# Kernel tuning notes

Measured on AMD Instinct MI355X. Metric: run time of the kernel, lower is better.

The kernel has to match this reference:

```python
import jax, jax.numpy as jnp
import numpy as np

B, N, DIM, H = 2, 2048, 1024, 16
D = DIM // H  # head_dim = 64


def setup_inputs() -> dict:
    key = jax.random.key(0)
    k1, k2, k3, k4, k5 = jax.random.split(key, 5)
    x = jax.random.normal(k1, (B, N, DIM), dtype=jnp.float32)
    # nn.Linear weights: [out_features, in_features]; scaled for stable softmax
    qkv_w = jax.random.normal(k2, (3 * DIM, DIM), dtype=jnp.float32) * (DIM ** -0.5)
    qkv_b = jax.random.normal(k3, (3 * DIM,), dtype=jnp.float32) * 0.02
    proj_w = jax.random.normal(k4, (DIM, DIM), dtype=jnp.float32) * (DIM ** -0.5)
    proj_b = jax.random.normal(k5, (DIM,), dtype=jnp.float32) * 0.02
    return {"x": x, "qkv_w": qkv_w, "qkv_b": qkv_b, "proj_w": proj_w, "proj_b": proj_b}


def reference(x, qkv_w, qkv_b, proj_w, proj_b):
    b, n, c = x.shape
    # qkv linear: [B,N,3C] -> [B,N,3,H,D] -> q,k,v each [B,H,N,D]
    qkv = x @ qkv_w.T + qkv_b
    qkv = qkv.reshape(b, n, 3, H, D).transpose(2, 0, 3, 1, 4)
    q, k, v = qkv[0], qkv[1], qkv[2]
    # scaled dot-product attention (no dropout, no mask); qk_norm=False, rope=None
    scale = D ** -0.5
    scores = jnp.einsum("bhqd,bhkd->bhqk", q, k) * scale
    attn = jax.nn.softmax(scores, axis=-1)
    out = jnp.einsum("bhqk,bhkd->bhqd", attn, v)
    # [B,H,N,D] -> [B,N,C]
    out = out.transpose(0, 2, 1, 3).reshape(b, n, c)
    # output projection
    return out @ proj_w.T + proj_b
```

## Files before the change

### kernel.cpp

```cpp
#include <hip/hip_runtime.h>
#include <hip/hip_bf16.h>
#include <math.h>

typedef __attribute__((ext_vector_type(8))) short short8v;
typedef __attribute__((ext_vector_type(4))) float f32x4;
typedef unsigned short ushort_t;

__device__ __forceinline__ ushort_t to_bf16(float v) {
    __hip_bfloat16 h = __float2bfloat16(v);
    return *(ushort_t*)&h;
}

__device__ __forceinline__ unsigned cvt_pk_bf16(float a, float b) {
    unsigned r;
    asm("v_cvt_pk_bf16_f32 %0, %1, %2" : "=v"(r) : "v"(a), "v"(b));
    return r;
}

__device__ __forceinline__ void load_lds_16B(const void* g, void* l) {
    __builtin_amdgcn_global_load_lds(
        (__attribute__((address_space(1))) unsigned int*)(g),
        (__attribute__((address_space(3))) unsigned int*)(l), 16, 0, 0);
}

__global__ __launch_bounds__(256) void convert_kernel(
    const float* __restrict__ x, const float* __restrict__ wq,
    const float* __restrict__ wp, ushort_t* __restrict__ xb,
    ushort_t* __restrict__ wqb, ushort_t* __restrict__ wpb)
{
    int c = blockIdx.x * 256 + threadIdx.x;
    const float* src; ushort_t* dst; int base;
    if (c < 524288)      { src = x;  dst = xb;  base = c; }
    else if (c < 917504) { src = wq; dst = wqb; base = c - 524288; }
    else                 { src = wp; dst = wpb; base = c - 917504; }
    const float4* s4 = (const float4*)src;
    float4 a = s4[2 * (size_t)base], b = s4[2 * (size_t)base + 1];
    float vals[8] = {a.x, a.y, a.z, a.w, b.x, b.y, b.z, b.w};
    short8v o;
#pragma unroll
    for (int j = 0; j < 8; j++) o[j] = (short)to_bf16(vals[j]);
    *(short8v*)(dst + 8 * (size_t)base) = o;
}

template <int MODE, int BM, int BN>
__global__ __launch_bounds__(256) void gemm_bf16_kernel(
    const ushort_t* __restrict__ A, const ushort_t* __restrict__ Bw,
    const float* __restrict__ bias, ushort_t* __restrict__ Qb,
    ushort_t* __restrict__ Kb, ushort_t* __restrict__ Vt,
    float* __restrict__ Cout)
{
    constexpr int MT = BM / 32, NT = BN / 32;
    __shared__ __align__(16) ushort_t As[BM * 32];
    __shared__ __align__(16) ushort_t Bs[BN * 32];
    const int t = threadIdx.x;
    const int w = t >> 6, l = t & 63;
    const int lo = l & 15, hi = l >> 4;
    const int wr = w >> 1, wc = w & 1;
    const int m0 = blockIdx.y * BM, n0 = blockIdx.x * BN;
    const int K = 1024;

    const ushort_t* ga = A + (size_t)(m0 + (t >> 2)) * K + (t & 3) * 8;
    const ushort_t* gb = Bw + (size_t)(n0 + (t >> 2)) * K + (t & 3) * 8;

    f32x4 acc[MT][NT] = {};

    for (int k0 = 0; k0 < 1024; k0 += 32) {
#pragma unroll
        for (int i = 0; i < BM / 64; i++)
            load_lds_16B(ga + (size_t)(i * 64) * K + k0, As + (i * 256 + w * 64) * 8);
#pragma unroll
        for (int i = 0; i < BN / 64; i++)
            load_lds_16B(gb + (size_t)(i * 64) * K + k0, Bs + (i * 256 + w * 64) * 8);
        __syncthreads();

        short8v af[MT], bf[NT];
#pragma unroll
        for (int mt = 0; mt < MT; mt++) {
            int r = wr * (BM / 2) + mt * 16 + lo;
            af[mt] = *(const short8v*)&As[r * 32 + hi * 8];
        }
#pragma unroll
        for (int nt = 0; nt < NT; nt++) {
            int r = wc * (BN / 2) + nt * 16 + lo;
            bf[nt] = *(const short8v*)&Bs[r * 32 + hi * 8];
        }
#pragma unroll
        for (int mt = 0; mt < MT; mt++)
#pragma unroll
            for (int nt = 0; nt < NT; nt++)
                acc[mt][nt] = __builtin_amdgcn_mfma_f32_16x16x32_bf16(
                    af[mt], bf[nt], acc[mt][nt], 0, 0, 0);
        __syncthreads();
    }

#pragma unroll
    for (int mt = 0; mt < MT; mt++) {
#pragma unroll
        for (int nt = 0; nt < NT; nt++) {
            int col = n0 + wc * (BN / 2) + nt * 16 + lo;
            float bv = bias[col];
#pragma unroll
            for (int reg = 0; reg < 4; reg++) {
                int row = m0 + wr * (BM / 2) + mt * 16 + hi * 4 + reg;
                float val = acc[mt][nt][reg] + bv;
                if constexpr (MODE == 0) {
                    int bb = row >> 11, n = row & 2047;
                    int which = col >> 10, rem = col & 1023;
                    int h = rem >> 6, d = rem & 63;
                    int bh = bb * 16 + h;
                    if (which == 0)
                        Qb[((size_t)bh * 2048 + n) * 64 + d] = to_bf16(val * 0.1803368601f);
                    else if (which == 1)
                        Kb[((size_t)bh * 2048 + n) * 64 + d] = to_bf16(val);
                    else
                        Vt[((size_t)bh * 64 + d) * 2048 + n] = to_bf16(val);
                } else {
                    Cout[(size_t)row * 1024 + col] = val;
                }
            }
        }
    }
}

__global__ __launch_bounds__(256) void attn_mfma_kernel(
    const ushort_t* __restrict__ Qg0, const ushort_t* __restrict__ Kg0,
    const ushort_t* __restrict__ Vg0, ushort_t* __restrict__ O)
{
    __shared__ __align__(16) ushort_t Ks[2 * 64 * 64];
    __shared__ __align__(16) ushort_t Vs[2 * 64 * 64];
    __shared__ __align__(16) ushort_t Ps[64 * 64];

    const int t = threadIdx.x;
    const int l = t & 63, w = t >> 6;
    const int lo = l & 15, hi = l >> 4;
    const int lin = (blockIdx.x & 7) * 128 + (blockIdx.x >> 3);
    const int bh = lin >> 5;
    const int q0 = (lin & 31) * 64;
    const ushort_t* Qg = Qg0 + (size_t)bh * 2048 * 64;
    const ushort_t* Kg = Kg0 + (size_t)bh * 2048 * 64;
    const ushort_t* Vg = Vg0 + (size_t)bh * 64 * 2048;

    short8v aq[2];
    {
        const ushort_t* qrow = Qg + (size_t)(q0 + w * 16 + lo) * 64;
        aq[0] = *(const short8v*)(qrow + hi * 8);
        aq[1] = *(const short8v*)(qrow + 32 + hi * 8);
    }

    const int srow = t >> 3, sg = t & 7;
    const int sgs = sg ^ (srow & 7);
    short8v rk0, rk1, rv0, rv1;

    f32x4 o_acc[4] = {};
    float m_i = -INFINITY, l_i = 0.0f;

    {
        rk0 = *(const short8v*)(Kg + (size_t)srow * 64 + sg * 8);
        rk1 = *(const short8v*)(Kg + (size_t)(srow + 32) * 64 + sg * 8);
        rv0 = *(const short8v*)(Vg + (size_t)srow * 2048 + sg * 8);
        rv1 = *(const short8v*)(Vg + (size_t)(srow + 32) * 2048 + sg * 8);
        *(short8v*)&Ks[srow * 64 + sgs * 8] = rk0;
        *(short8v*)&Ks[(srow + 32) * 64 + sgs * 8] = rk1;
        *(short8v*)&Vs[srow * 64 + sgs * 8] = rv0;
        *(short8v*)&Vs[(srow + 32) * 64 + sgs * 8] = rv1;
    }
    __syncthreads();

    for (int kt = 0; kt < 32; kt++) {
        const int bufo = (kt & 1) * 4096;
        if (kt < 31) {
            const int k0n = (kt + 1) * 64;
            rk0 = *(const short8v*)(Kg + (size_t)(k0n + srow) * 64 + sg * 8);
            rk1 = *(const short8v*)(Kg + (size_t)(k0n + srow + 32) * 64 + sg * 8);
            rv0 = *(const short8v*)(Vg + (size_t)srow * 2048 + k0n + sg * 8);
            rv1 = *(const short8v*)(Vg + (size_t)(srow + 32) * 2048 + k0n + sg * 8);
        }

        f32x4 s_acc[4];
        __builtin_amdgcn_s_setprio(1);
#pragma unroll
        for (int nt = 0; nt < 4; nt++) {
            f32x4 acc = {0.f, 0.f, 0.f, 0.f};
#pragma unroll
            for (int kk = 0; kk < 2; kk++) {
                int r = nt * 16 + lo;
                int g = (kk * 4 + hi) ^ (r & 7);
                short8v ak = *(const short8v*)&Ks[bufo + r * 64 + g * 8];
                acc = __builtin_amdgcn_mfma_f32_16x16x32_bf16(ak, aq[kk], acc, 0, 0, 0);
            }
            s_acc[nt] = acc;
        }
        __builtin_amdgcn_s_setprio(0);

        float pmax = fmaxf(
            fmaxf(fmaxf(fmaxf(s_acc[0][0], s_acc[0][1]), fmaxf(s_acc[0][2], s_acc[0][3])),
                  fmaxf(fmaxf(s_acc[1][0], s_acc[1][1]), fmaxf(s_acc[1][2], s_acc[1][3]))),
            fmaxf(fmaxf(fmaxf(s_acc[2][0], s_acc[2][1]), fmaxf(s_acc[2][2], s_acc[2][3])),
                  fmaxf(fmaxf(s_acc[3][0], s_acc[3][1]), fmaxf(s_acc[3][2], s_acc[3][3]))));
        pmax = fmaxf(pmax, __shfl_xor(pmax, 16));
        pmax = fmaxf(pmax, __shfl_xor(pmax, 32));

        if (__any(pmax > m_i + 11.0f)) {
            float mnew = fmaxf(m_i, pmax);
            float al = __builtin_amdgcn_exp2f(m_i - mnew);
            m_i = mnew;
            l_i *= al;
            float a0 = __shfl(al, hi * 4 + 0);
            float a1 = __shfl(al, hi * 4 + 1);
            float a2 = __shfl(al, hi * 4 + 2);
            float a3 = __shfl(al, hi * 4 + 3);
#pragma unroll
            for (int dt = 0; dt < 4; dt++) {
                o_acc[dt][0] *= a0; o_acc[dt][1] *= a1;
                o_acc[dt][2] *= a2; o_acc[dt][3] *= a3;
            }
        }

        float p[4][4];
        float ps = 0.0f;
#pragma unroll
        for (int nt = 0; nt < 4; nt++)
#pragma unroll
            for (int reg = 0; reg < 4; reg++) {
                p[nt][reg] = __builtin_amdgcn_exp2f(s_acc[nt][reg] - m_i);
                ps += p[nt][reg];
            }
        ps += __shfl_xor(ps, 16);
        ps += __shfl_xor(ps, 32);
        l_i += ps;

        const int R = w * 16 + lo;
#pragma unroll
        for (int nt = 0; nt < 4; nt++) {
            int c0 = nt * 16 + hi * 4;
            int g = (c0 >> 3) ^ (R & 7);
            uint2 pv = {cvt_pk_bf16(p[nt][0], p[nt][1]),
                        cvt_pk_bf16(p[nt][2], p[nt][3])};
            *(uint2*)&Ps[R * 64 + g * 8 + (c0 & 7)] = pv;
        }
        asm volatile("s_waitcnt lgkmcnt(0)" ::: "memory");
        short8v pa0 = *(const short8v*)&Ps[R * 64 + ((0 + hi) ^ (R & 7)) * 8];
        short8v pa1 = *(const short8v*)&Ps[R * 64 + ((4 + hi) ^ (R & 7)) * 8];

        if (kt < 31) {
            const int nxto = 4096 - bufo;
            *(short8v*)&Ks[nxto + srow * 64 + sgs * 8] = rk0;
            *(short8v*)&Ks[nxto + (srow + 32) * 64 + sgs * 8] = rk1;
            *(short8v*)&Vs[nxto + srow * 64 + sgs * 8] = rv0;
            *(short8v*)&Vs[nxto + (srow + 32) * 64 + sgs * 8] = rv1;
        }

        __builtin_amdgcn_s_setprio(1);
#pragma unroll
        for (int dt = 0; dt < 4; dt++) {
            int r = dt * 16 + lo;
            short8v bv0 = *(const short8v*)&Vs[bufo + r * 64 + ((0 + hi) ^ (r & 7)) * 8];
            short8v bv1 = *(const short8v*)&Vs[bufo + r * 64 + ((4 + hi) ^ (r & 7)) * 8];
            o_acc[dt] = __builtin_amdgcn_mfma_f32_16x16x32_bf16(pa0, bv0, o_acc[dt], 0, 0, 0);
            o_acc[dt] = __builtin_amdgcn_mfma_f32_16x16x32_bf16(pa1, bv1, o_acc[dt], 0, 0, 0);
        }
        __builtin_amdgcn_s_setprio(0);
        __syncthreads();
    }

    const int b = bh >> 4, h = bh & 15;
#pragma unroll
    for (int reg = 0; reg < 4; reg++) {
        float lv = __shfl(l_i, hi * 4 + reg);
        float inv = 1.0f / lv;
        int row = q0 + w * 16 + hi * 4 + reg;
        ushort_t* orow = O + ((size_t)(b * 2048 + row)) * 1024 + h * 64;
#pragma unroll
        for (int dt = 0; dt < 4; dt++)
            orow[dt * 16 + lo] = to_bf16(o_acc[dt][reg] * inv);
    }
}

extern "C" void kernel_launch(void* const* d_in, const int* in_sizes, int n_in,
                              void* d_out, int out_size, void* d_ws, size_t ws_size,
                              hipStream_t stream) {
    const float* x      = (const float*)d_in[0];
    const float* qkv_w  = (const float*)d_in[1];
    const float* qkv_b  = (const float*)d_in[2];
    const float* proj_w = (const float*)d_in[3];
    const float* proj_b = (const float*)d_in[4];
    float* out = (float*)d_out;

    ushort_t* xb  = (ushort_t*)d_ws;
    ushort_t* wqb = xb  + 4194304;
    ushort_t* wpb = wqb + 3145728;
    ushort_t* qb  = wpb + 1048576;
    ushort_t* kb  = qb  + 4194304;
    ushort_t* vt  = kb  + 4194304;
    ushort_t* aob = vt  + 4194304;

    convert_kernel<<<4096, 256, 0, stream>>>(x, qkv_w, proj_w, xb, wqb, wpb);
    gemm_bf16_kernel<0, 128, 128><<<dim3(24, 32), 256, 0, stream>>>(
        xb, wqb, qkv_b, qb, kb, vt, nullptr);
    attn_mfma_kernel<<<1024, 256, 0, stream>>>(qb, kb, vt, aob);
    gemm_bf16_kernel<1, 128, 128><<<dim3(8, 32), 256, 0, stream>>>(
        aob, wpb, proj_b, nullptr, nullptr, nullptr, out);
}
```

Baseline: 142.6 us.

## Double GEMM K-tile with swizzled LDS; keep P in registers via permuted V layout

The GEMM kernel now stages 64-wide K tiles in LDS with an XOR swizzle, which halves the number of barrier-separated iterations and reduces bank conflicts. The attention kernel drops the LDS round-trip for the softmax probabilities P. The bf16-packed P values are used directly as MFMA A operands, and V is written to LDS in a permuted, swizzled order so its key dimension lines up with the register layout P already has. This removes an LDS store, a wait and two reads per tile, at the cost of more complex V store addressing using 8-byte writes.

```diff
diff --git a/kernel.cpp b/kernel.cpp
--- a/kernel.cpp
+++ b/kernel.cpp
@@ -50,8 +50,8 @@
     float* __restrict__ Cout)
 {
     constexpr int MT = BM / 32, NT = BN / 32;
-    __shared__ __align__(16) ushort_t As[BM * 32];
-    __shared__ __align__(16) ushort_t Bs[BN * 32];
+    __shared__ __align__(16) ushort_t As[BM * 64];
+    __shared__ __align__(16) ushort_t Bs[BN * 64];
     const int t = threadIdx.x;
     const int w = t >> 6, l = t & 63;
     const int lo = l & 15, hi = l >> 4;
@@ -59,37 +59,45 @@
     const int m0 = blockIdx.y * BM, n0 = blockIdx.x * BN;
     const int K = 1024;
 
-    const ushort_t* ga = A + (size_t)(m0 + (t >> 2)) * K + (t & 3) * 8;
-    const ushort_t* gb = Bw + (size_t)(n0 + (t >> 2)) * K + (t & 3) * 8;
+    const int srow = t >> 3;
+    const int schk = (t & 7) ^ (srow & 7);
+    const ushort_t* ga = A + (size_t)(m0 + srow) * K + schk * 8;
+    const ushort_t* gb = Bw + (size_t)(n0 + srow) * K + schk * 8;
 
     f32x4 acc[MT][NT] = {};
 
-    for (int k0 = 0; k0 < 1024; k0 += 32) {
-#pragma unroll
-        for (int i = 0; i < BM / 64; i++)
-            load_lds_16B(ga + (size_t)(i * 64) * K + k0, As + (i * 256 + w * 64) * 8);
-#pragma unroll
-        for (int i = 0; i < BN / 64; i++)
-            load_lds_16B(gb + (size_t)(i * 64) * K + k0, Bs + (i * 256 + w * 64) * 8);
+    for (int k0 = 0; k0 < 1024; k0 += 64) {
+#pragma unroll
+        for (int i = 0; i < BM / 32; i++)
+            load_lds_16B(ga + (size_t)(i * 32) * K + k0, As + (i * 32 + w * 8) * 64);
+#pragma unroll
+        for (int i = 0; i < BN / 32; i++)
+            load_lds_16B(gb + (size_t)(i * 32) * K + k0, Bs + (i * 32 + w * 8) * 64);
         __syncthreads();
 
-        short8v af[MT], bf[NT];
+        short8v af[MT][2], bf[NT][2];
 #pragma unroll
         for (int mt = 0; mt < MT; mt++) {
             int r = wr * (BM / 2) + mt * 16 + lo;
-            af[mt] = *(const short8v*)&As[r * 32 + hi * 8];
+#pragma unroll
+            for (int kk = 0; kk < 2; kk++)
+                af[mt][kk] = *(const short8v*)&As[r * 64 + ((kk * 4 + hi) ^ (r & 7)) * 8];
         }
 #pragma unroll
         for (int nt = 0; nt < NT; nt++) {
             int r = wc * (BN / 2) + nt * 16 + lo;
-            bf[nt] = *(const short8v*)&Bs[r * 32 + hi * 8];
-        }
-#pragma unroll
-        for (int mt = 0; mt < MT; mt++)
-#pragma unroll
-            for (int nt = 0; nt < NT; nt++)
-                acc[mt][nt] = __builtin_amdgcn_mfma_f32_16x16x32_bf16(
-                    af[mt], bf[nt], acc[mt][nt], 0, 0, 0);
+#pragma unroll
+            for (int kk = 0; kk < 2; kk++)
+                bf[nt][kk] = *(const short8v*)&Bs[r * 64 + ((kk * 4 + hi) ^ (r & 7)) * 8];
+        }
+#pragma unroll
+        for (int kk = 0; kk < 2; kk++)
+#pragma unroll
+            for (int mt = 0; mt < MT; mt++)
+#pragma unroll
+                for (int nt = 0; nt < NT; nt++)
+                    acc[mt][nt] = __builtin_amdgcn_mfma_f32_16x16x32_bf16(
+                        af[mt][kk], bf[nt][kk], acc[mt][nt], 0, 0, 0);
         __syncthreads();
     }
 
@@ -128,7 +136,6 @@
 {
     __shared__ __align__(16) ushort_t Ks[2 * 64 * 64];
     __shared__ __align__(16) ushort_t Vs[2 * 64 * 64];
-    __shared__ __align__(16) ushort_t Ps[64 * 64];
 
     const int t = threadIdx.x;
     const int l = t & 63, w = t >> 6;
@@ -149,20 +156,27 @@
 
     const int srow = t >> 3, sg = t & 7;
     const int sgs = sg ^ (srow & 7);
-    short8v rk0, rk1, rv0, rv1;
+    const int gv0 = (sg >> 2) * 4 + (sg & 1) * 2;
+    const int vo = ((sg >> 1) & 1) * 4;
+    const int vswz0 = srow & 7;
+    uint4 rk0, rk1, rv0, rv1;
 
     f32x4 o_acc[4] = {};
     float m_i = -INFINITY, l_i = 0.0f;
 
     {
-        rk0 = *(const short8v*)(Kg + (size_t)srow * 64 + sg * 8);
-        rk1 = *(const short8v*)(Kg + (size_t)(srow + 32) * 64 + sg * 8);
-        rv0 = *(const short8v*)(Vg + (size_t)srow * 2048 + sg * 8);
-        rv1 = *(const short8v*)(Vg + (size_t)(srow + 32) * 2048 + sg * 8);
-        *(short8v*)&Ks[srow * 64 + sgs * 8] = rk0;
-        *(short8v*)&Ks[(srow + 32) * 64 + sgs * 8] = rk1;
-        *(short8v*)&Vs[srow * 64 + sgs * 8] = rv0;
-        *(short8v*)&Vs[(srow + 32) * 64 + sgs * 8] = rv1;
+        rk0 = *(const uint4*)(Kg + (size_t)srow * 64 + sg * 8);
+        rk1 = *(const uint4*)(Kg + (size_t)(srow + 32) * 64 + sg * 8);
+        rv0 = *(const uint4*)(Vg + (size_t)srow * 2048 + sg * 8);
+        rv1 = *(const uint4*)(Vg + (size_t)(srow + 32) * 2048 + sg * 8);
+        *(uint4*)&Ks[srow * 64 + sgs * 8] = rk0;
+        *(uint4*)&Ks[(srow + 32) * 64 + sgs * 8] = rk1;
+        uint2 a0 = {rv0.x, rv0.y}, b0 = {rv0.z, rv0.w};
+        uint2 a1 = {rv1.x, rv1.y}, b1 = {rv1.z, rv1.w};
+        *(uint2*)&Vs[srow * 64 + (gv0 ^ vswz0) * 8 + vo] = a0;
+        *(uint2*)&Vs[srow * 64 + ((gv0 + 1) ^ vswz0) * 8 + vo] = b0;
+        *(uint2*)&Vs[(srow + 32) * 64 + (gv0 ^ vswz0) * 8 + vo] = a1;
+        *(uint2*)&Vs[(srow + 32) * 64 + ((gv0 + 1) ^ vswz0) * 8 + vo] = b1;
     }
     __syncthreads();
 
@@ -170,10 +184,10 @@
         const int bufo = (kt & 1) * 4096;
         if (kt < 31) {
             const int k0n = (kt + 1) * 64;
-            rk0 = *(const short8v*)(Kg + (size_t)(k0n + srow) * 64 + sg * 8);
-            rk1 = *(const short8v*)(Kg + (size_t)(k0n + srow + 32) * 64 + sg * 8);
-            rv0 = *(const short8v*)(Vg + (size_t)srow * 2048 + k0n + sg * 8);
-            rv1 = *(const short8v*)(Vg + (size_t)(srow + 32) * 2048 + k0n + sg * 8);
+            rk0 = *(const uint4*)(Kg + (size_t)(k0n + srow) * 64 + sg * 8);
+            rk1 = *(const uint4*)(Kg + (size_t)(k0n + srow + 32) * 64 + sg * 8);
+            rv0 = *(const uint4*)(Vg + (size_t)srow * 2048 + k0n + sg * 8);
+            rv1 = *(const uint4*)(Vg + (size_t)(srow + 32) * 2048 + k0n + sg * 8);
         }
 
         f32x4 s_acc[4];
@@ -229,25 +243,27 @@
         ps += __shfl_xor(ps, 32);
         l_i += ps;
 
-        const int R = w * 16 + lo;
-#pragma unroll
-        for (int nt = 0; nt < 4; nt++) {
-            int c0 = nt * 16 + hi * 4;
-            int g = (c0 >> 3) ^ (R & 7);
-            uint2 pv = {cvt_pk_bf16(p[nt][0], p[nt][1]),
-                        cvt_pk_bf16(p[nt][2], p[nt][3])};
-            *(uint2*)&Ps[R * 64 + g * 8 + (c0 & 7)] = pv;
-        }
-        asm volatile("s_waitcnt lgkmcnt(0)" ::: "memory");
-        short8v pa0 = *(const short8v*)&Ps[R * 64 + ((0 + hi) ^ (R & 7)) * 8];
-        short8v pa1 = *(const short8v*)&Ps[R * 64 + ((4 + hi) ^ (R & 7)) * 8];
+        int4 w0i = {(int)cvt_pk_bf16(p[0][0], p[0][1]),
+                    (int)cvt_pk_bf16(p[0][2], p[0][3]),
+                    (int)cvt_pk_bf16(p[1][0], p[1][1]),
+                    (int)cvt_pk_bf16(p[1][2], p[1][3])};
+        int4 w1i = {(int)cvt_pk_bf16(p[2][0], p[2][1]),
+                    (int)cvt_pk_bf16(p[2][2], p[2][3]),
+                    (int)cvt_pk_bf16(p[3][0], p[3][1]),
+                    (int)cvt_pk_bf16(p[3][2], p[3][3])};
+        short8v pa0 = __builtin_bit_cast(short8v, w0i);
+        short8v pa1 = __builtin_bit_cast(short8v, w1i);
 
         if (kt < 31) {
             const int nxto = 4096 - bufo;
-            *(short8v*)&Ks[nxto + srow * 64 + sgs * 8] = rk0;
-            *(short8v*)&Ks[nxto + (srow + 32) * 64 + sgs * 8] = rk1;
-            *(short8v*)&Vs[nxto + srow * 64 + sgs * 8] = rv0;
-            *(short8v*)&Vs[nxto + (srow + 32) * 64 + sgs * 8] = rv1;
+            *(uint4*)&Ks[nxto + srow * 64 + sgs * 8] = rk0;
+            *(uint4*)&Ks[nxto + (srow + 32) * 64 + sgs * 8] = rk1;
+            uint2 a0 = {rv0.x, rv0.y}, b0 = {rv0.z, rv0.w};
+            uint2 a1 = {rv1.x, rv1.y}, b1 = {rv1.z, rv1.w};
+            *(uint2*)&Vs[nxto + srow * 64 + (gv0 ^ vswz0) * 8 + vo] = a0;
+            *(uint2*)&Vs[nxto + srow * 64 + ((gv0 + 1) ^ vswz0) * 8 + vo] = b0;
+            *(uint2*)&Vs[nxto + (srow + 32) * 64 + (gv0 ^ vswz0) * 8 + vo] = a1;
+            *(uint2*)&Vs[nxto + (srow + 32) * 64 + ((gv0 + 1) ^ vswz0) * 8 + vo] = b1;
         }
 
         __builtin_amdgcn_s_setprio(1);
```

Measured after the change: 148.7 us. 1.04x slower.

## Process 128 queries per attention block and keep P in registers

Applied to the files above, without the earlier changes.

Each wave now handles two 16-row query fragments, so the attention block covers 128 queries and the grid shrinks to 512 blocks. Every K/V tile staged in LDS is reused twice as much, halving global K/V traffic. The P tile no longer round-trips through shared memory: the V tile is written to LDS with a permuted column layout so the S accumulator registers can be packed straight into the MFMA A operand. In exchange, register pressure roughly doubles and there are fewer blocks to fill the CUs.

```diff
diff --git a/kernel.cpp b/kernel.cpp
--- a/kernel.cpp
+++ b/kernel.cpp
@@ -128,41 +128,49 @@
 {
     __shared__ __align__(16) ushort_t Ks[2 * 64 * 64];
     __shared__ __align__(16) ushort_t Vs[2 * 64 * 64];
-    __shared__ __align__(16) ushort_t Ps[64 * 64];
 
     const int t = threadIdx.x;
     const int l = t & 63, w = t >> 6;
     const int lo = l & 15, hi = l >> 4;
-    const int lin = (blockIdx.x & 7) * 128 + (blockIdx.x >> 3);
-    const int bh = lin >> 5;
-    const int q0 = (lin & 31) * 64;
+    const int lin = (blockIdx.x & 7) * 64 + (blockIdx.x >> 3);
+    const int bh = lin >> 4;
+    const int q0 = (lin & 15) * 128;
     const ushort_t* Qg = Qg0 + (size_t)bh * 2048 * 64;
     const ushort_t* Kg = Kg0 + (size_t)bh * 2048 * 64;
     const ushort_t* Vg = Vg0 + (size_t)bh * 64 * 2048;
 
-    short8v aq[2];
-    {
-        const ushort_t* qrow = Qg + (size_t)(q0 + w * 16 + lo) * 64;
-        aq[0] = *(const short8v*)(qrow + hi * 8);
-        aq[1] = *(const short8v*)(qrow + 32 + hi * 8);
+    short8v aq[2][2];
+#pragma unroll
+    for (int qf = 0; qf < 2; qf++) {
+        const ushort_t* qrow = Qg + (size_t)(q0 + w * 32 + qf * 16 + lo) * 64;
+        aq[qf][0] = *(const short8v*)(qrow + hi * 8);
+        aq[qf][1] = *(const short8v*)(qrow + 32 + hi * 8);
     }
 
     const int srow = t >> 3, sg = t & 7;
     const int sgs = sg ^ (srow & 7);
-    short8v rk0, rk1, rv0, rv1;
-
-    f32x4 o_acc[4] = {};
-    float m_i = -INFINITY, l_i = 0.0f;
+    const int gv0 = (sg >> 2) * 4 + (sg & 1) * 2;
+    const int vo = ((sg >> 1) & 1) * 4;
+    const int vswz0 = srow & 7;
+    uint4 rk0, rk1, rv0, rv1;
+
+    f32x4 o_acc[2][4] = {};
+    float m_i[2] = {-INFINITY, -INFINITY};
+    float l_i[2] = {0.0f, 0.0f};
 
     {
-        rk0 = *(const short8v*)(Kg + (size_t)srow * 64 + sg * 8);
-        rk1 = *(const short8v*)(Kg + (size_t)(srow + 32) * 64 + sg * 8);
-        rv0 = *(const short8v*)(Vg + (size_t)srow * 2048 + sg * 8);
-        rv1 = *(const short8v*)(Vg + (size_t)(srow + 32) * 2048 + sg * 8);
-        *(short8v*)&Ks[srow * 64 + sgs * 8] = rk0;
-        *(short8v*)&Ks[(srow + 32) * 64 + sgs * 8] = rk1;
-        *(short8v*)&Vs[srow * 64 + sgs * 8] = rv0;
-        *(short8v*)&Vs[(srow + 32) * 64 + sgs * 8] = rv1;
+        rk0 = *(const uint4*)(Kg + (size_t)srow * 64 + sg * 8);
+        rk1 = *(const uint4*)(Kg + (size_t)(srow + 32) * 64 + sg * 8);
+        rv0 = *(const uint4*)(Vg + (size_t)srow * 2048 + sg * 8);
+        rv1 = *(const uint4*)(Vg + (size_t)(srow + 32) * 2048 + sg * 8);
+        *(uint4*)&Ks[srow * 64 + sgs * 8] = rk0;
+        *(uint4*)&Ks[(srow + 32) * 64 + sgs * 8] = rk1;
+        uint2 va0 = {rv0.x, rv0.y}, vb0 = {rv0.z, rv0.w};
+        uint2 va1 = {rv1.x, rv1.y}, vb1 = {rv1.z, rv1.w};
+        *(uint2*)&Vs[srow * 64 + (gv0 ^ vswz0) * 8 + vo] = va0;
+        *(uint2*)&Vs[srow * 64 + ((gv0 + 1) ^ vswz0) * 8 + vo] = vb0;
+        *(uint2*)&Vs[(srow + 32) * 64 + (gv0 ^ vswz0) * 8 + vo] = va1;
+        *(uint2*)&Vs[(srow + 32) * 64 + ((gv0 + 1) ^ vswz0) * 8 + vo] = vb1;
     }
     __syncthreads();
 
@@ -170,84 +178,97 @@
         const int bufo = (kt & 1) * 4096;
         if (kt < 31) {
             const int k0n = (kt + 1) * 64;
-            rk0 = *(const short8v*)(Kg + (size_t)(k0n + srow) * 64 + sg * 8);
-            rk1 = *(const short8v*)(Kg + (size_t)(k0n + srow + 32) * 64 + sg * 8);
-            rv0 = *(const short8v*)(Vg + (size_t)srow * 2048 + k0n + sg * 8);
-            rv1 = *(const short8v*)(Vg + (size_t)(srow + 32) * 2048 + k0n + sg * 8);
-        }
-
-        f32x4 s_acc[4];
+            rk0 = *(const uint4*)(Kg + (size_t)(k0n + srow) * 64 + sg * 8);
+            rk1 = *(const uint4*)(Kg + (size_t)(k0n + srow + 32) * 64 + sg * 8);
+            rv0 = *(const uint4*)(Vg + (size_t)srow * 2048 + k0n + sg * 8);
+            rv1 = *(const uint4*)(Vg + (size_t)(srow + 32) * 2048 + k0n + sg * 8);
+        }
+
+        f32x4 s_acc[2][4];
         __builtin_amdgcn_s_setprio(1);
 #pragma unroll
         for (int nt = 0; nt < 4; nt++) {
-            f32x4 acc = {0.f, 0.f, 0.f, 0.f};
+            f32x4 acc0 = {0.f, 0.f, 0.f, 0.f};
+            f32x4 acc1 = {0.f, 0.f, 0.f, 0.f};
 #pragma unroll
             for (int kk = 0; kk < 2; kk++) {
                 int r = nt * 16 + lo;
                 int g = (kk * 4 + hi) ^ (r & 7);
                 short8v ak = *(const short8v*)&Ks[bufo + r * 64 + g * 8];
-                acc = __builtin_amdgcn_mfma_f32_16x16x32_bf16(ak, aq[kk], acc, 0, 0, 0);
+                acc0 = __builtin_amdgcn_mfma_f32_16x16x32_bf16(ak, aq[0][kk], acc0, 0, 0, 0);
+                acc1 = __builtin_amdgcn_mfma_f32_16x16x32_bf16(ak, aq[1][kk], acc1, 0, 0, 0);
             }
-            s_acc[nt] = acc;
+            s_acc[0][nt] = acc0;
+            s_acc[1][nt] = acc1;
         }
         __builtin_amdgcn_s_setprio(0);
 
-        float pmax = fmaxf(
-            fmaxf(fmaxf(fmaxf(s_acc[0][0], s_acc[0][1]), fmaxf(s_acc[0][2], s_acc[0][3])),
-                  fmaxf(fmaxf(s_acc[1][0], s_acc[1][1]), fmaxf(s_acc[1][2], s_acc[1][3]))),
-            fmaxf(fmaxf(fmaxf(s_acc[2][0], s_acc[2][1]), fmaxf(s_acc[2][2], s_acc[2][3])),
-                  fmaxf(fmaxf(s_acc[3][0], s_acc[3][1]), fmaxf(s_acc[3][2], s_acc[3][3]))));
-        pmax = fmaxf(pmax, __shfl_xor(pmax, 16));
-        pmax = fmaxf(pmax, __shfl_xor(pmax, 32));
-
-        if (__any(pmax > m_i + 11.0f)) {
-            float mnew = fmaxf(m_i, pmax);
-            float al = __builtin_amdgcn_exp2f(m_i - mnew);
-            m_i = mnew;
-            l_i *= al;
-            float a0 = __shfl(al, hi * 4 + 0);
-            float a1 = __shfl(al, hi * 4 + 1);
-            float a2 = __shfl(al, hi * 4 + 2);
-            float a3 = __shfl(al, hi * 4 + 3);
-#pragma unroll
-            for (int dt = 0; dt < 4; dt++) {
-                o_acc[dt][0] *= a0; o_acc[dt][1] *= a1;
-                o_acc[dt][2] *= a2; o_acc[dt][3] *= a3;
+        short8v pa[2][2];
+#pragma unroll
+        for (int qf = 0; qf < 2; qf++) {
+            float pm = fmaxf(
+                fmaxf(fmaxf(fmaxf(s_acc[qf][0][0], s_acc[qf][0][1]),
+                            fmaxf(s_acc[qf][0][2], s_acc[qf][0][3])),
+                      fmaxf(fmaxf(s_acc[qf][1][0], s_acc[qf][1][1]),
+                            fmaxf(s_acc[qf][1][2], s_acc[qf][1][3]))),
+                fmaxf(fmaxf(fmaxf(s_acc[qf][2][0], s_acc[qf][2][1]),
+                            fmaxf(s_acc[qf][2][2], s_acc[qf][2][3])),
+                      fmaxf(fmaxf(s_acc[qf][3][0], s_acc[qf][3][1]),
+                            fmaxf(s_acc[qf][3][2], s_acc[qf][3][3]))));
+            pm = fmaxf(pm, __shfl_xor(pm, 16));
+            pm = fmaxf(pm, __shfl_xor(pm, 32));
+
+            if (__any(pm > m_i[qf] + 11.0f)) {
+                float mnew = fmaxf(m_i[qf], pm);
+                float al = __builtin_amdgcn_exp2f(m_i[qf] - mnew);
+                m_i[qf] = mnew;
+                l_i[qf] *= al;
+                float a0 = __shfl(al, hi * 4 + 0);
+                float a1 = __shfl(al, hi * 4 + 1);
+                float a2 = __shfl(al, hi * 4 + 2);
+                float a3 = __shfl(al, hi * 4 + 3);
+#pragma unroll
+                for (int dt = 0; dt < 4; dt++) {
+                    o_acc[qf][dt][0] *= a0; o_acc[qf][dt][1] *= a1;
+                    o_acc[qf][dt][2] *= a2; o_acc[qf][dt][3] *= a3;
+                }
             }
-        }
-
-        float p[4][4];
-        float ps = 0.0f;
-#pragma unroll
-        for (int nt = 0; nt < 4; nt++)
-#pragma unroll
-            for (int reg = 0; reg < 4; reg++) {
-                p[nt][reg] = __builtin_amdgcn_exp2f(s_acc[nt][reg] - m_i);
-                ps += p[nt][reg];
-            }
-        ps += __shfl_xor(ps, 16);
-        ps += __shfl_xor(ps, 32);
-        l_i += ps;
-
-        const int R = w * 16 + lo;
-#pragma unroll
-        for (int nt = 0; nt < 4; nt++) {
-            int c0 = nt * 16 + hi * 4;
-            int g = (c0 >> 3) ^ (R & 7);
-            uint2 pv = {cvt_pk_bf16(p[nt][0], p[nt][1]),
-                        cvt_pk_bf16(p[nt][2], p[nt][3])};
-            *(uint2*)&Ps[R * 64 + g * 8 + (c0 & 7)] = pv;
-        }
-        asm volatile("s_waitcnt lgkmcnt(0)" ::: "memory");
-        short8v pa0 = *(const short8v*)&Ps[R * 64 + ((0 + hi) ^ (R & 7)) * 8];
-        short8v pa1 = *(const short8v*)&Ps[R * 64 + ((4 + hi) ^ (R & 7)) * 8];
+
+            float ps = 0.0f;
+#pragma unroll
+            for (int nt = 0; nt < 4; nt++)
+#pragma unroll
+                for (int reg = 0; reg < 4; reg++) {
+                    s_acc[qf][nt][reg] =
+                        __builtin_amdgcn_exp2f(s_acc[qf][nt][reg] - m_i[qf]);
+                    ps += s_acc[qf][nt][reg];
+                }
+            ps += __shfl_xor(ps, 16);
+            ps += __shfl_xor(ps, 32);
+            l_i[qf] += ps;
+
+            int4 w0i = {(int)cvt_pk_bf16(s_acc[qf][0][0], s_acc[qf][0][1]),
+                        (int)cvt_pk_bf16(s_acc[qf][0][2], s_acc[qf][0][3]),
+                        (int)cvt_pk_bf16(s_acc[qf][1][0], s_acc[qf][1][1]),
+                        (int)cvt_pk_bf16(s_acc[qf][1][2], s_acc[qf][1][3])};
+            int4 w1i = {(int)cvt_pk_bf16(s_acc[qf][2][0], s_acc[qf][2][1]),
+                        (int)cvt_pk_bf16(s_acc[qf][2][2], s_acc[qf][2][3]),
+                        (int)cvt_pk_bf16(s_acc[qf][3][0], s_acc[qf][3][1]),
+                        (int)cvt_pk_bf16(s_acc[qf][3][2], s_acc[qf][3][3])};
+            pa[qf][0] = __builtin_bit_cast(short8v, w0i);
+            pa[qf][1] = __builtin_bit_cast(short8v, w1i);
+        }
 
         if (kt < 31) {
             const int nxto = 4096 - bufo;
-            *(short8v*)&Ks[nxto + srow * 64 + sgs * 8] = rk0;
-            *(short8v*)&Ks[nxto + (srow + 32) * 64 + sgs * 8] = rk1;
-            *(short8v*)&Vs[nxto + srow * 64 + sgs * 8] = rv0;
-            *(short8v*)&Vs[nxto + (srow + 32) * 64 + sgs * 8] = rv1;
+            *(uint4*)&Ks[nxto + srow * 64 + sgs * 8] = rk0;
+            *(uint4*)&Ks[nxto + (srow + 32) * 64 + sgs * 8] = rk1;
+            uint2 va0 = {rv0.x, rv0.y}, vb0 = {rv0.z, rv0.w};
+            uint2 va1 = {rv1.x, rv1.y}, vb1 = {rv1.z, rv1.w};
+            *(uint2*)&Vs[nxto + srow * 64 + (gv0 ^ vswz0) * 8 + vo] = va0;
+            *(uint2*)&Vs[nxto + srow * 64 + ((gv0 + 1) ^ vswz0) * 8 + vo] = vb0;
+            *(uint2*)&Vs[nxto + (srow + 32) * 64 + (gv0 ^ vswz0) * 8 + vo] = va1;
+            *(uint2*)&Vs[nxto + (srow + 32) * 64 + ((gv0 + 1) ^ vswz0) * 8 + vo] = vb1;
         }
 
         __builtin_amdgcn_s_setprio(1);
@@ -256,8 +277,10 @@
             int r = dt * 16 + lo;
             short8v bv0 = *(const short8v*)&Vs[bufo + r * 64 + ((0 + hi) ^ (r & 7)) * 8];
             short8v bv1 = *(const short8v*)&Vs[bufo + r * 64 + ((4 + hi) ^ (r & 7)) * 8];
-            o_acc[dt] = __builtin_amdgcn_mfma_f32_16x16x32_bf16(pa0, bv0, o_acc[dt], 0, 0, 0);
-            o_acc[dt] = __builtin_amdgcn_mfma_f32_16x16x32_bf16(pa1, bv1, o_acc[dt], 0, 0, 0);
+            o_acc[0][dt] = __builtin_amdgcn_mfma_f32_16x16x32_bf16(pa[0][0], bv0, o_acc[0][dt], 0, 0, 0);
+            o_acc[0][dt] = __builtin_amdgcn_mfma_f32_16x16x32_bf16(pa[0][1], bv1, o_acc[0][dt], 0, 0, 0);
+            o_acc[1][dt] = __builtin_amdgcn_mfma_f32_16x16x32_bf16(pa[1][0], bv0, o_acc[1][dt], 0, 0, 0);
+            o_acc[1][dt] = __builtin_amdgcn_mfma_f32_16x16x32_bf16(pa[1][1], bv1, o_acc[1][dt], 0, 0, 0);
         }
         __builtin_amdgcn_s_setprio(0);
         __syncthreads();
@@ -265,14 +288,17 @@
 
     const int b = bh >> 4, h = bh & 15;
 #pragma unroll
-    for (int reg = 0; reg < 4; reg++) {
-        float lv = __shfl(l_i, hi * 4 + reg);
-        float inv = 1.0f / lv;
-        int row = q0 + w * 16 + hi * 4 + reg;
-        ushort_t* orow = O + ((size_t)(b * 2048 + row)) * 1024 + h * 64;
-#pragma unroll
-        for (int dt = 0; dt < 4; dt++)
-            orow[dt * 16 + lo] = to_bf16(o_acc[dt][reg] * inv);
+    for (int qf = 0; qf < 2; qf++) {
+#pragma unroll
+        for (int reg = 0; reg < 4; reg++) {
+            float lv = __shfl(l_i[qf], hi * 4 + reg);
+            float inv = 1.0f / lv;
+            int row = q0 + w * 32 + qf * 16 + hi * 4 + reg;
+            ushort_t* orow = O + ((size_t)(b * 2048 + row)) * 1024 + h * 64;
+#pragma unroll
+            for (int dt = 0; dt < 4; dt++)
+                orow[dt * 16 + lo] = to_bf16(o_acc[qf][dt][reg] * inv);
+        }
     }
 }
 
@@ -297,7 +323,7 @@
     convert_kernel<<<4096, 256, 0, stream>>>(x, qkv_w, proj_w, xb, wqb, wpb);
     gemm_bf16_kernel<0, 128, 128><<<dim3(24, 32), 256, 0, stream>>>(
         xb, wqb, qkv_b, qb, kb, vt, nullptr);
-    attn_mfma_kernel<<<1024, 256, 0, stream>>>(qb, kb, vt, aob);
+    attn_mfma_kernel<<<512, 256, 0, stream>>>(qb, kb, vt, aob);
     gemm_bf16_kernel<1, 128, 128><<<dim3(8, 32), 256, 0, stream>>>(
         aob, wpb, proj_b, nullptr, nullptr, nullptr, out);
 }
```

Result: faster. 131.9 us (-7.5%).
